# Kernel optimization log

Measured on AMD Instinct MI355X. Metric: run time of the kernel, lower is better.

The kernel has to match this reference:

```python
import jax, jax.numpy as jnp
import numpy as np

D = 512
SCALE = 1.0 / np.sqrt(D).astype(np.float32)


def setup_inputs() -> dict:
    key = jax.random.key(0)
    ks = jax.random.split(key, 6)
    B, S = 8, 2048
    x = jax.random.normal(ks[0], (B, S, D), dtype=jnp.float32)
    bias = jax.random.normal(ks[1], (1,), dtype=jnp.float32)
    key_padding_mask = jax.random.randint(ks[2], (B, S), 0, 2).astype(jnp.bool_)
    # nn.Linear weights, stored as [out, in]; y = x @ W.T
    Wq = jax.random.normal(ks[3], (D, D), dtype=jnp.float32) * (1.0 / np.sqrt(D))
    Wk = jax.random.normal(ks[4], (D, D), dtype=jnp.float32) * (1.0 / np.sqrt(D))
    Wv = jax.random.normal(ks[5], (D, D), dtype=jnp.float32) * (1.0 / np.sqrt(D))
    return {"x": x, "bias": bias, "key_padding_mask": key_padding_mask,
            "Wq": Wq, "Wk": Wk, "Wv": Wv}


def reference(x, bias, key_padding_mask, Wq, Wk, Wv):
    # Projections (Linear without bias): [B,S,D] @ [D,D]^T
    Q = jnp.einsum('bsd,ed->bse', x, Wq)
    K = jnp.einsum('bsd,ed->bse', x, Wk)
    V = jnp.einsum('bsd,ed->bse', x, Wv)
    # Scaled scores with additive scalar bias: [B,S,S]
    scores = jnp.einsum('bqd,bkd->bqk', Q, K) * SCALE + bias
    # Key padding mask: mask keys (last dim) with -inf
    scores = jnp.where(key_padding_mask[:, None, :], -jnp.inf, scores)
    attn = jax.nn.softmax(scores, axis=-1)
    attn = jnp.nan_to_num(attn, nan=0.0)  # fully-masked rows -> 0
    # Dropout is inference no-op
    return jnp.einsum('bqk,bkd->bqd', attn, V)
```

## Files before the change

kernel.cpp:

```cpp
#include <hip/hip_runtime.h>

typedef short bf16x8 __attribute__((ext_vector_type(8)));
typedef float f32x4 __attribute__((ext_vector_type(4)));
typedef float f32x16 __attribute__((ext_vector_type(16)));

__device__ __forceinline__ ushort f2bf(float f) {
    union { float f; unsigned u; } v; v.f = f;
    unsigned r = (v.u + 0x7fffu + ((v.u >> 16) & 1u)) >> 16;
    return (ushort)r;
}
__device__ __forceinline__ float bf2f(ushort u) {
    union { unsigned u; float f; } v; v.u = ((unsigned)u) << 16;
    return v.f;
}
__device__ __forceinline__ void async_copy16(void* lds, const void* g) {
    __builtin_amdgcn_global_load_lds(
        (const __attribute__((address_space(1))) unsigned*)g,
        (__attribute__((address_space(3))) unsigned*)lds, 16, 0, 0);
}

__global__ __launch_bounds__(256)
void prep_kernel(const float* __restrict__ x, const float* __restrict__ Wq,
                 const float* __restrict__ Wk, const float* __restrict__ Wv,
                 const int* __restrict__ mask,
                 ushort* __restrict__ xb, ushort* __restrict__ wqT,
                 ushort* __restrict__ wkT, ushort* __restrict__ wvb,
                 int* __restrict__ idx, int* __restrict__ cnt)
{
    const int bid = blockIdx.x, t = threadIdx.x;
    if (bid < 8192) {
        int i = (bid * 256 + t) * 4;
        float4 v = *(const float4*)(x + i);
        ushort4 o;
        o.x = f2bf(v.x); o.y = f2bf(v.y); o.z = f2bf(v.z); o.w = f2bf(v.w);
        *(ushort4*)(xb + i) = o;
    } else if (bid < 8320) {
        __shared__ ushort T[64][72];
        int r = bid - 8192;
        const int z = r >> 6; r &= 63;
        const float* in = z ? Wk : Wq;
        ushort* out     = z ? wkT : wqT;
        const int r0 = (r >> 3) * 64, c0 = (r & 7) * 64;
        const int rr = t >> 3, cc8 = (t & 7) * 8;
        #pragma unroll
        for (int pass = 0; pass < 2; ++pass) {
            int rw = rr + pass * 32;
            float4 a = *(const float4*)(in + (size_t)(r0 + rw) * 512 + c0 + cc8);
            float4 bq = *(const float4*)(in + (size_t)(r0 + rw) * 512 + c0 + cc8 + 4);
            T[rw][cc8+0]=f2bf(a.x);  T[rw][cc8+1]=f2bf(a.y);  T[rw][cc8+2]=f2bf(a.z);  T[rw][cc8+3]=f2bf(a.w);
            T[rw][cc8+4]=f2bf(bq.x); T[rw][cc8+5]=f2bf(bq.y); T[rw][cc8+6]=f2bf(bq.z); T[rw][cc8+7]=f2bf(bq.w);
        }
        __syncthreads();
        const int c = t >> 2, seg = (t & 3) * 16;
        ushort tmp[16];
        #pragma unroll
        for (int j = 0; j < 16; ++j) tmp[j] = T[seg + j][c];
        *(uint4*)(out + (size_t)(c0 + c) * 512 + r0 + seg)     = *(uint4*)&tmp[0];
        *(uint4*)(out + (size_t)(c0 + c) * 512 + r0 + seg + 8) = *(uint4*)&tmp[8];
    } else if (bid < 8576) {
        int i = ((bid - 8320) * 256 + t) * 4;
        float4 v = *(const float4*)(Wv + i);
        ushort4 o;
        o.x = f2bf(v.x); o.y = f2bf(v.y); o.z = f2bf(v.z); o.w = f2bf(v.w);
        *(ushort4*)(wvb + i) = o;
    } else {
        __shared__ int sc[256];
        int seg = bid - 8576, b = seg >> 1, half = seg & 1;
        const int* m = mask + b * 2048 + half * 1024;
        int v0 = (m[t*4+0] == 0), v1 = (m[t*4+1] == 0);
        int v2 = (m[t*4+2] == 0), v3 = (m[t*4+3] == 0);
        int c = v0 + v1 + v2 + v3;
        sc[t] = c; __syncthreads();
        for (int ofs = 1; ofs < 256; ofs <<= 1) {
            int xx = (t >= ofs) ? sc[t - ofs] : 0;
            __syncthreads(); sc[t] += xx; __syncthreads();
        }
        int pos = sc[t] - c + seg * 1024;
        if (v0) idx[pos++] = t*4+0;
        if (v1) idx[pos++] = t*4+1;
        if (v2) idx[pos++] = t*4+2;
        if (v3) idx[pos++] = t*4+3;
        if (t == 255) cnt[seg] = sc[255];
    }
}

__global__ __launch_bounds__(256)
void gather_cvt(const float* __restrict__ x, const int* __restrict__ idx,
                const int* __restrict__ cnt, ushort* __restrict__ xc)
{
    int seg = blockIdx.x, b = seg >> 1, half = seg & 1;
    int n = cnt[seg];
    int wave = threadIdx.x >> 6, lane = threadIdx.x & 63;
    int j0 = blockIdx.y * 64 + wave * 16;
    for (int i = 0; i < 16; ++i) {
        int j = j0 + i;
        uint4 val = {0u, 0u, 0u, 0u};
        if (j < n) {
            int src = idx[seg * 1024 + j];
            const float* r = x + ((size_t)(b * 2048 + half * 1024 + src)) * 512 + lane * 8;
            float4 a = *(const float4*)r, c4 = *(const float4*)(r + 4);
            ushort tmp[8];
            tmp[0]=f2bf(a.x); tmp[1]=f2bf(a.y); tmp[2]=f2bf(a.z); tmp[3]=f2bf(a.w);
            tmp[4]=f2bf(c4.x); tmp[5]=f2bf(c4.y); tmp[6]=f2bf(c4.z); tmp[7]=f2bf(c4.w);
            val = *(uint4*)tmp;
        }
        *(uint4*)(xc + ((size_t)(seg * 1024 + j)) * 512 + lane * 8) = val;
    }
}

__device__ __forceinline__ void gemm_core(const ushort* __restrict__ A,
                                          const ushort* __restrict__ B,
                                          ushort* __restrict__ C,
                                          int N, int K, int mBase, int nBase)
{
    __shared__ ushort As[128][32];
    __shared__ ushort Bs[128][32];
    const int tid = threadIdx.x;
    const int lane = tid & 63, wave = tid >> 6;
    const int wm = wave >> 1, wn = wave & 1;
    const int lr = lane & 15, lq = lane >> 4;
    const int sr = lane >> 2;
    const int sc = (lane & 3) * 8;

    f32x4 acc[4][4];
    #pragma unroll
    for (int i = 0; i < 4; ++i)
        #pragma unroll
        for (int j = 0; j < 4; ++j) acc[i][j] = (f32x4){0.f, 0.f, 0.f, 0.f};

    for (int k0 = 0; k0 < K; k0 += 32) {
        __syncthreads();
        #pragma unroll
        for (int j = 0; j < 2; ++j) {
            int rbase = wave * 32 + j * 16;
            async_copy16(&As[rbase][0], A + (size_t)(mBase + rbase + sr) * K + k0 + sc);
            async_copy16(&Bs[rbase][0], B + (size_t)(nBase + rbase + sr) * K + k0 + sc);
        }
        __syncthreads();
        bf16x8 af[4], bfr[4];
        #pragma unroll
        for (int mi = 0; mi < 4; ++mi) af[mi] = *(const bf16x8*)&As[wm * 64 + mi * 16 + lr][lq * 8];
        #pragma unroll
        for (int ni = 0; ni < 4; ++ni) bfr[ni] = *(const bf16x8*)&Bs[wn * 64 + ni * 16 + lr][lq * 8];
        #pragma unroll
        for (int mi = 0; mi < 4; ++mi)
            #pragma unroll
            for (int ni = 0; ni < 4; ++ni)
                acc[mi][ni] = __builtin_amdgcn_mfma_f32_16x16x32_bf16(af[mi], bfr[ni], acc[mi][ni], 0, 0, 0);
    }
    #pragma unroll
    for (int mi = 0; mi < 4; ++mi)
        #pragma unroll
        for (int ni = 0; ni < 4; ++ni)
            #pragma unroll
            for (int r = 0; r < 4; ++r) {
                int m = mBase + wm * 64 + mi * 16 + lq * 4 + r;
                int n = nBase + wn * 64 + ni * 16 + lr;
                C[(size_t)m * N + n] = f2bf(acc[mi][ni][r]);
            }
}

__global__ __launch_bounds__(256, 2)
void gemm_m(const ushort* __restrict__ A, const ushort* __restrict__ B,
            ushort* __restrict__ C) {
    gemm_core(A, B, C, 512, 512, blockIdx.y * 128, blockIdx.x * 128);
}

__global__ __launch_bounds__(256, 2)
void gemm_kv(const ushort* __restrict__ xc, const ushort* __restrict__ Mb,
             ushort* __restrict__ Kc, const ushort* __restrict__ wv,
             ushort* __restrict__ Vtc, const int* __restrict__ cnt)
{
    const ushort *A, *B; ushort* C; int N, mBase, nBase;
    if (blockIdx.z == 0) {
        mBase = blockIdx.y * 128; nBase = blockIdx.x * 128;
        if ((mBase & 1023) >= cnt[mBase >> 10]) return;
        A = xc; B = Mb; C = Kc; N = 512;
    } else {
        mBase = blockIdx.x * 128; nBase = blockIdx.y * 128;
        if ((nBase & 1023) >= cnt[nBase >> 10]) return;
        A = wv; B = xc; C = Vtc; N = 16384;
    }
    gemm_core(A, B, C, N, 512, mBase, nBase);
}

__global__ __launch_bounds__(256, 2)
void attn_kernel(const ushort* __restrict__ Qg, const ushort* __restrict__ Kcg,
                 const ushort* __restrict__ Vtcg, const int* __restrict__ cntg,
                 ushort* __restrict__ Pog, float* __restrict__ Mlg)
{
    const int S = 2048;
    const float SL2E = 0.0637587160f;

    __shared__ ushort Ks[32][548];
    __shared__ ushort Vs[512][36];
    __shared__ ushort Ps[2][32][36];

    const int b = blockIdx.y, qt = blockIdx.x, half = blockIdx.z;
    const int seg = b * 2 + half;
    const int tid = threadIdx.x, lane = tid & 63, wave = tid >> 6;
    const int lr = lane & 15, lq = lane >> 4;
    const int p = wave >> 1, s = wave & 1;
    const int l32 = lane & 31, lh = lane >> 5;

    const int n = cntg[seg];
    const int ntiles = (n + 31) >> 5;

    const ushort* Qp = Qg + ((size_t)b * S + qt * 64 + wave * 16 + lr) * 512;
    bf16x8 qf[16];
    #pragma unroll
    for (int c = 0; c < 16; ++c) qf[c] = *(const bf16x8*)(Qp + c * 32 + lq * 8);

    f32x16 o[8];
    #pragma unroll
    for (int i = 0; i < 8; ++i)
        #pragma unroll
        for (int r = 0; r < 16; ++r) o[i][r] = 0.f;
    float l_i[4] = {0.f, 0.f, 0.f, 0.f};

    const char* Kseg = (const char*)(Kcg + (size_t)seg * 1024 * 512);
    const char* Vseg = (const char*)Vtcg + (size_t)(seg * 1024) * 2;

    for (int kt = 0; kt < ntiles; ++kt) {
        const int key0 = kt * 32;
        __syncthreads();
        {
            const char* gK = Kseg + (size_t)key0 * 1024;
            #pragma unroll
            for (int i = 0; i < 8; ++i) {
                int row = wave * 8 + i;
                async_copy16(&Ks[row][0], gK + (size_t)row * 1024 + lane * 16);
            }
        }
        const bool va0 = (key0 + lr) < n;
        const bool va1 = (key0 + 16 + lr) < n;
        __syncthreads();
        uint4 vreg[8];
        {
            const char* gV = Vseg + (size_t)key0 * 2;
            #pragma unroll
            for (int i = 0; i < 8; ++i) {
                int off = i * 4096 + tid * 16;
                int row = off >> 6, col = off & 63;
                vreg[i] = *(const uint4*)(gV + (size_t)row * 32768 + col);
            }
        }
        f32x4 sf0 = (f32x4){0.f,0.f,0.f,0.f}, sf1 = (f32x4){0.f,0.f,0.f,0.f};
        #pragma unroll
        for (int ks = 0; ks < 16; ++ks) {
            bf16x8 kf0 = *(const bf16x8*)&Ks[lr][ks * 32 + lq * 8];
            bf16x8 kf1 = *(const bf16x8*)&Ks[16 + lr][ks * 32 + lq * 8];
            sf0 = __builtin_amdgcn_mfma_f32_16x16x32_bf16(qf[ks], kf0, sf0, 0, 0, 0);
            sf1 = __builtin_amdgcn_mfma_f32_16x16x32_bf16(qf[ks], kf1, sf1, 0, 0, 0);
        }
        #pragma unroll
        for (int r = 0; r < 4; ++r) {
            float p0 = va0 ? exp2f(fmaf(sf0[r], SL2E, -8.f)) : 0.f;
            float p1 = va1 ? exp2f(fmaf(sf1[r], SL2E, -8.f)) : 0.f;
            l_i[r] += p0 + p1;
            Ps[p][16 * s + lq * 4 + r][lr]      = f2bf(p0);
            Ps[p][16 * s + lq * 4 + r][16 + lr] = f2bf(p1);
        }
        #pragma unroll
        for (int i = 0; i < 8; ++i) {
            int off = i * 4096 + tid * 16;
            int row = off >> 6, col = off & 63;
            *(uint4*)((char*)Vs + row * 72 + col) = vreg[i];
        }
        __syncthreads();
        bf16x8 pA0 = *(const bf16x8*)&Ps[p][l32][lh * 8];
        bf16x8 pA1 = *(const bf16x8*)&Ps[p][l32][16 + lh * 8];
        #pragma unroll
        for (int dt = 0; dt < 8; ++dt) {
            int d = s * 256 + dt * 32 + l32;
            bf16x8 v0 = *(const bf16x8*)&Vs[d][lh * 8];
            bf16x8 v1 = *(const bf16x8*)&Vs[d][16 + lh * 8];
            o[dt] = __builtin_amdgcn_mfma_f32_32x32x16_bf16(pA0, v0, o[dt], 0, 0, 0);
            o[dt] = __builtin_amdgcn_mfma_f32_32x32x16_bf16(pA1, v1, o[dt], 0, 0, 0);
        }
    }
    #pragma unroll
    for (int r = 0; r < 4; ++r)
        #pragma unroll
        for (int off = 1; off < 16; off <<= 1)
            l_i[r] += __shfl_xor(l_i[r], off, 16);
    const size_t growbase = (size_t)half * 16384 + (size_t)b * S + qt * 64;
    if (lr == 0) {
        #pragma unroll
        for (int r = 0; r < 4; ++r)
            Mlg[growbase + wave * 16 + lq * 4 + r] = l_i[r];
    }
    ushort* Pop = Pog + (growbase + p * 32) * 512;
    #pragma unroll
    for (int dt = 0; dt < 8; ++dt) {
        int ocol = s * 256 + dt * 32 + l32;
        #pragma unroll
        for (int r = 0; r < 16; ++r) {
            int orow = (r & 3) + 8 * (r >> 2) + 4 * lh;
            Pop[(size_t)orow * 512 + ocol] = f2bf(o[dt][r]);
        }
    }
}

__global__ __launch_bounds__(256)
void combine_kernel(const ushort* __restrict__ Po, const float* __restrict__ Ml,
                    float* __restrict__ out)
{
    int i = (blockIdx.x * 256 + threadIdx.x) * 4;
    int row = i >> 9;
    float l = Ml[row] + Ml[16384 + row];
    float s = l > 0.f ? 1.f / l : 0.f;
    ushort4 p1 = *(const ushort4*)(Po + i);
    ushort4 p2 = *(const ushort4*)(Po + 8388608 + i);
    float4 o;
    o.x = (bf2f(p1.x) + bf2f(p2.x)) * s;
    o.y = (bf2f(p1.y) + bf2f(p2.y)) * s;
    o.z = (bf2f(p1.z) + bf2f(p2.z)) * s;
    o.w = (bf2f(p1.w) + bf2f(p2.w)) * s;
    *(float4*)(out + i) = o;
}

extern "C" void kernel_launch(void* const* d_in, const int* in_sizes, int n_in,
                              void* d_out, int out_size, void* d_ws, size_t ws_size,
                              hipStream_t stream) {
    const float* x  = (const float*)d_in[0];
    const int* mask = (const int*)d_in[2];
    const float* Wq = (const float*)d_in[3];
    const float* Wk = (const float*)d_in[4];
    const float* Wv = (const float*)d_in[5];
    float* out = (float*)d_out;

    ushort* ws   = (ushort*)d_ws;
    ushort* xb   = ws;
    ushort* wqT  = ws + 8388608;
    ushort* wkT  = wqT + 262144;
    ushort* wvb  = wkT + 262144;
    ushort* xc   = ws + 9175040;
    ushort* Pob  = ws + 9175040;
    ushort* Mb   = ws + 17563648;
    int*    idxb = (int*)(ws + 17825792);
    ushort* Kc   = ws + 25952256;
    ushort* Vtc  = ws + 34340864;
    float*  Mlb  = (float*)(ws + 42729472);
    int*    cntb = (int*)(ws + 42795008);

    prep_kernel<<<8592, 256, 0, stream>>>(x, Wq, Wk, Wv, mask,
                                          xb, wqT, wkT, wvb, idxb, cntb);
    gather_cvt<<<dim3(16, 16), 256, 0, stream>>>(x, idxb, cntb, xc);
    gemm_m<<<dim3(4, 4), 256, 0, stream>>>(wqT, wkT, Mb);
    gemm_kv<<<dim3(4, 128, 2), 256, 0, stream>>>(xc, Mb, Kc, wvb, Vtc, cntb);
    attn_kernel<<<dim3(32, 8, 2), 256, 0, stream>>>(xb, Kc, Vtc, cntb, Pob, Mlb);
    combine_kernel<<<8192, 256, 0, stream>>>(Pob, Mlb, out);
}
```

Measured before the change: 228.6 us.

## Prefetch K tiles into registers, remap block order, and relax LDS barriers

K tiles are now loaded into registers one iteration ahead and written to LDS by each thread, replacing async global-to-LDS copies issued after a barrier. This aims to hide global latency behind the QK and PV MFMAs. The block index is remapped so that consecutive blocks span different segments. Barriers become lgkmcnt-wait plus s_barrier, which skips waiting on outstanding global loads, and the QK accumulation is split into two independent chains. MFMA sections are raised with s_setprio. Holding the K prefetch in registers adds register pressure, which may lower occupancy.

```diff
diff --git a/kernel.cpp b/kernel.cpp
--- a/kernel.cpp
+++ b/kernel.cpp
@@ -17,6 +17,9 @@
     __builtin_amdgcn_global_load_lds(
         (const __attribute__((address_space(1))) unsigned*)g,
         (__attribute__((address_space(3))) unsigned*)lds, 16, 0, 0);
+}
+__device__ __forceinline__ void lds_barrier() {
+    asm volatile("s_waitcnt lgkmcnt(0)\n\ts_barrier" ::: "memory");
 }
 
 __global__ __launch_bounds__(256)
@@ -196,8 +199,11 @@
     __shared__ ushort Vs[512][36];
     __shared__ ushort Ps[2][32][36];
 
-    const int b = blockIdx.y, qt = blockIdx.x, half = blockIdx.z;
-    const int seg = b * 2 + half;
+    const int lin = blockIdx.x + 32 * blockIdx.y + 256 * blockIdx.z;
+    const int seg = (lin & 7) * 2 + (lin >> 8);
+    const int qt  = (lin >> 3) & 31;
+    const int b = seg >> 1, half = seg & 1;
+
     const int tid = threadIdx.x, lane = tid & 63, wave = tid >> 6;
     const int lr = lane & 15, lq = lane >> 4;
     const int p = wave >> 1, s = wave & 1;
@@ -221,42 +227,57 @@
     const char* Kseg = (const char*)(Kcg + (size_t)seg * 1024 * 512);
     const char* Vseg = (const char*)Vtcg + (size_t)(seg * 1024) * 2;
 
+    uint4 kreg[8];
+    #pragma unroll
+    for (int i = 0; i < 8; ++i)
+        kreg[i] = *(const uint4*)(Kseg + i * 4096 + tid * 16);
+
     for (int kt = 0; kt < ntiles; ++kt) {
         const int key0 = kt * 32;
-        __syncthreads();
-        {
-            const char* gK = Kseg + (size_t)key0 * 1024;
-            #pragma unroll
-            for (int i = 0; i < 8; ++i) {
-                int row = wave * 8 + i;
-                async_copy16(&Ks[row][0], gK + (size_t)row * 1024 + lane * 16);
-            }
-        }
-        const bool va0 = (key0 + lr) < n;
-        const bool va1 = (key0 + 16 + lr) < n;
-        __syncthreads();
+        lds_barrier();
+        #pragma unroll
+        for (int i = 0; i < 8; ++i) {
+            int off = i * 4096 + tid * 16;
+            *(uint4*)((char*)Ks + (off >> 10) * 1096 + (off & 1023)) = kreg[i];
+        }
         uint4 vreg[8];
         {
             const char* gV = Vseg + (size_t)key0 * 2;
             #pragma unroll
             for (int i = 0; i < 8; ++i) {
                 int off = i * 4096 + tid * 16;
-                int row = off >> 6, col = off & 63;
-                vreg[i] = *(const uint4*)(gV + (size_t)row * 32768 + col);
+                vreg[i] = *(const uint4*)(gV + (size_t)(off >> 6) * 32768 + (off & 63));
             }
         }
-        f32x4 sf0 = (f32x4){0.f,0.f,0.f,0.f}, sf1 = (f32x4){0.f,0.f,0.f,0.f};
-        #pragma unroll
-        for (int ks = 0; ks < 16; ++ks) {
-            bf16x8 kf0 = *(const bf16x8*)&Ks[lr][ks * 32 + lq * 8];
-            bf16x8 kf1 = *(const bf16x8*)&Ks[16 + lr][ks * 32 + lq * 8];
-            sf0 = __builtin_amdgcn_mfma_f32_16x16x32_bf16(qf[ks], kf0, sf0, 0, 0, 0);
-            sf1 = __builtin_amdgcn_mfma_f32_16x16x32_bf16(qf[ks], kf1, sf1, 0, 0, 0);
-        }
+        if (kt + 1 < ntiles) {
+            const char* gK = Kseg + (size_t)(key0 + 32) * 1024;
+            #pragma unroll
+            for (int i = 0; i < 8; ++i)
+                kreg[i] = *(const uint4*)(gK + i * 4096 + tid * 16);
+        }
+        const bool va0 = (key0 + lr) < n;
+        const bool va1 = (key0 + 16 + lr) < n;
+        lds_barrier();
+        f32x4 sA = (f32x4){0.f,0.f,0.f,0.f}, sB = (f32x4){0.f,0.f,0.f,0.f};
+        f32x4 sC = (f32x4){0.f,0.f,0.f,0.f}, sD = (f32x4){0.f,0.f,0.f,0.f};
+        __builtin_amdgcn_s_setprio(1);
+        #pragma unroll
+        for (int ks = 0; ks < 16; ks += 2) {
+            bf16x8 kf0a = *(const bf16x8*)&Ks[lr][ks * 32 + lq * 8];
+            bf16x8 kf1a = *(const bf16x8*)&Ks[16 + lr][ks * 32 + lq * 8];
+            bf16x8 kf0b = *(const bf16x8*)&Ks[lr][(ks + 1) * 32 + lq * 8];
+            bf16x8 kf1b = *(const bf16x8*)&Ks[16 + lr][(ks + 1) * 32 + lq * 8];
+            sA = __builtin_amdgcn_mfma_f32_16x16x32_bf16(qf[ks], kf0a, sA, 0, 0, 0);
+            sB = __builtin_amdgcn_mfma_f32_16x16x32_bf16(qf[ks], kf1a, sB, 0, 0, 0);
+            sC = __builtin_amdgcn_mfma_f32_16x16x32_bf16(qf[ks + 1], kf0b, sC, 0, 0, 0);
+            sD = __builtin_amdgcn_mfma_f32_16x16x32_bf16(qf[ks + 1], kf1b, sD, 0, 0, 0);
+        }
+        __builtin_amdgcn_s_setprio(0);
         #pragma unroll
         for (int r = 0; r < 4; ++r) {
-            float p0 = va0 ? exp2f(fmaf(sf0[r], SL2E, -8.f)) : 0.f;
-            float p1 = va1 ? exp2f(fmaf(sf1[r], SL2E, -8.f)) : 0.f;
+            float s0 = sA[r] + sC[r], s1 = sB[r] + sD[r];
+            float p0 = va0 ? exp2f(fmaf(s0, SL2E, -8.f)) : 0.f;
+            float p1 = va1 ? exp2f(fmaf(s1, SL2E, -8.f)) : 0.f;
             l_i[r] += p0 + p1;
             Ps[p][16 * s + lq * 4 + r][lr]      = f2bf(p0);
             Ps[p][16 * s + lq * 4 + r][16 + lr] = f2bf(p1);
@@ -267,9 +288,10 @@
             int row = off >> 6, col = off & 63;
             *(uint4*)((char*)Vs + row * 72 + col) = vreg[i];
         }
-        __syncthreads();
+        lds_barrier();
         bf16x8 pA0 = *(const bf16x8*)&Ps[p][l32][lh * 8];
         bf16x8 pA1 = *(const bf16x8*)&Ps[p][l32][16 + lh * 8];
+        __builtin_amdgcn_s_setprio(1);
         #pragma unroll
         for (int dt = 0; dt < 8; ++dt) {
             int d = s * 256 + dt * 32 + l32;
@@ -278,6 +300,7 @@
             o[dt] = __builtin_amdgcn_mfma_f32_32x32x16_bf16(pA0, v0, o[dt], 0, 0, 0);
             o[dt] = __builtin_amdgcn_mfma_f32_32x32x16_bf16(pA1, v1, o[dt], 0, 0, 0);
         }
+        __builtin_amdgcn_s_setprio(0);
     }
     #pragma unroll
     for (int r = 0; r < 4; ++r)
```

Measured after the change: 311.7 us. 1.36x slower.
